# Performance work log

Measured on AMD Instinct MI355X. Metric: run time of the kernel, lower is better.

Reference implementation:

```python
import jax, jax.numpy as jnp
import numpy as np

N_NODES = 50000
N_EDGES = 500000
D_IN, D_HID = 128, 256


def _add_self_loops(edge_index, n):
    loop = jnp.arange(n, dtype=edge_index.dtype)
    src = jnp.concatenate([edge_index[0], loop])
    dst = jnp.concatenate([edge_index[1], loop])
    return src, dst


def _gcn_layer(x, W, b, src, dst, dinv_sqrt, n):
    # x: [N, d_in] -> h: [N, d_out]
    h = x @ W
    # symmetric normalization D^{-1/2} (A+I) D^{-1/2}
    norm = dinv_sqrt[src] * dinv_sqrt[dst]          # [E+N]
    msg = h[src] * norm[:, None]                    # gather + scale
    agg = jax.ops.segment_sum(msg, dst, num_segments=n)  # scatter-add
    return agg + b


def setup_inputs() -> dict:
    key = jax.random.key(0)
    ks = jax.random.split(key, 8)
    x = jax.random.normal(ks[0], (N_NODES, D_IN), dtype=jnp.float32)
    edge_index = jax.random.randint(ks[1], (2, N_EDGES), 0, N_NODES, dtype=jnp.int64 if jax.config.read('jax_enable_x64') else jnp.int32)
    s = lambda fan_in: 1.0 / np.sqrt(fan_in)
    W1 = jax.random.uniform(ks[2], (D_IN, D_HID), jnp.float32, -s(D_IN), s(D_IN))
    b1 = jnp.zeros((D_HID,), jnp.float32)
    W2 = jax.random.uniform(ks[3], (D_HID, D_HID), jnp.float32, -s(D_HID), s(D_HID))
    b2 = jnp.zeros((D_HID,), jnp.float32)
    W3 = jax.random.uniform(ks[4], (D_HID, D_HID), jnp.float32, -s(D_HID), s(D_HID))
    b3 = jnp.zeros((D_HID,), jnp.float32)
    return {"x": x, "edge_index": edge_index, "W1": W1, "b1": b1,
            "W2": W2, "b2": b2, "W3": W3, "b3": b3}


def reference(x, edge_index, W1, b1, W2, b2, W3, b3):
    n = x.shape[0]
    src, dst = _add_self_loops(edge_index, n)
    # degree includes self loops (edge weight 1), as in torch_geometric GCNConv
    deg = jax.ops.segment_sum(jnp.ones_like(dst, dtype=x.dtype), dst, num_segments=n)
    dinv_sqrt = jnp.where(deg > 0, jax.lax.rsqrt(jnp.maximum(deg, 1e-12)), 0.0)
    h = jax.nn.relu(_gcn_layer(x, W1, b1, src, dst, dinv_sqrt, n))
    h = jax.nn.relu(_gcn_layer(h, W2, b2, src, dst, dinv_sqrt, n))
    h = _gcn_layer(h, W3, b3, src, dst, dinv_sqrt, n)
    return h
```

## Files before the change

### kernel.cpp

```cpp
#include <hip/hip_runtime.h>

#define NNODES 50000
#define NEDGES 500000
#define DIN 128
#define DHID 256
#define MPAD 50048
#define NI4 12500
#define NSB 49

typedef unsigned short u16;
typedef __attribute__((ext_vector_type(8))) _Float16 half8;
typedef __attribute__((ext_vector_type(4))) float f32x4;

__device__ __forceinline__ u16 f2h(float f) {
  union { _Float16 h; u16 u; } v; v.h = (_Float16)f; return v.u;
}
__device__ __forceinline__ float h2f(unsigned int u) {
  union { _Float16 h; u16 u; } v; v.u = (u16)u; return (float)v.h;
}

#define GLDS16(g, l) __builtin_amdgcn_global_load_lds( \
    (const __attribute__((address_space(1))) void*)(g), \
    (__attribute__((address_space(3))) void*)(l), 16, 0, 0)

__global__ void k_zero_i32(int* __restrict__ p, int n) {
  int i = blockIdx.x * blockDim.x + threadIdx.x;
  if (i < n) p[i] = 0;
}

__global__ void k_hist(const int* __restrict__ dst, int* __restrict__ deg, int e) {
  int i = blockIdx.x * blockDim.x + threadIdx.x;
  if (i < e) atomicAdd(&deg[dst[i]], 1);
}

__global__ __launch_bounds__(256) void k_blocksum(const int* __restrict__ deg,
                                                  int* __restrict__ partials) {
  __shared__ int red[256];
  int tid = threadIdx.x;
  int t4 = blockIdx.x * 256 + tid;
  int sum = 0;
  if (t4 < NI4) {
    int4 v = ((const int4*)deg)[t4];
    sum = v.x + v.y + v.z + v.w;
  }
  red[tid] = sum;
  __syncthreads();
  for (int off = 128; off > 0; off >>= 1) {
    if (tid < off) red[tid] += red[tid + off];
    __syncthreads();
  }
  if (tid == 0) partials[blockIdx.x] = red[0];
}

__global__ __launch_bounds__(256) void k_scan2(int* __restrict__ deg,
                                               const int* __restrict__ partials,
                                               int* __restrict__ row_ptr,
                                               float* __restrict__ dinv) {
  __shared__ int sdata[256];
  __shared__ int sprefix;
  int tid = threadIdx.x, bid = blockIdx.x;
  int t4 = bid * 256 + tid;
  int4 v = make_int4(0, 0, 0, 0);
  if (t4 < NI4) v = ((const int4*)deg)[t4];
  int tsum = v.x + v.y + v.z + v.w;
  sdata[tid] = tsum;
  if (tid == 0) {
    int pre = 0;
    for (int b = 0; b < bid; ++b) pre += partials[b];
    sprefix = pre;
  }
  __syncthreads();
  for (int off = 1; off < 256; off <<= 1) {
    int val = (tid >= off) ? sdata[tid - off] : 0;
    __syncthreads();
    sdata[tid] += val;
    __syncthreads();
  }
  if (t4 < NI4) {
    int run = sdata[tid] - tsum + sprefix;
    int base = t4 * 4;
    float4 dv;
    dv.x = rsqrtf((float)v.x + 1.0f);
    dv.y = rsqrtf((float)v.y + 1.0f);
    dv.z = rsqrtf((float)v.z + 1.0f);
    dv.w = rsqrtf((float)v.w + 1.0f);
    *(float4*)(dinv + base) = dv;
    row_ptr[base + 0] = run; run += v.x;
    row_ptr[base + 1] = run; run += v.y;
    row_ptr[base + 2] = run; run += v.z;
    row_ptr[base + 3] = run; run += v.w;
    if (base + 4 == NNODES) row_ptr[NNODES] = run;
    ((int4*)deg)[t4] = make_int4(0, 0, 0, 0);
  }
}

__global__ void k_fill(const int* __restrict__ src, const int* __restrict__ dst,
                       const float* __restrict__ dinv, const int* __restrict__ row_ptr,
                       int* __restrict__ cursor, int* __restrict__ csr_src,
                       float* __restrict__ csr_nrm, int e) {
  int i = blockIdx.x * blockDim.x + threadIdx.x;
  if (i < e) {
    int d = dst[i], s = src[i];
    int pos = row_ptr[d] + atomicAdd(&cursor[d], 1);
    csr_src[pos] = s;
    csr_nrm[pos] = dinv[s] * dinv[d];
  }
}

__global__ void k_x2f16(const float* __restrict__ x, u16* __restrict__ xh, int total4) {
  int i = blockIdx.x * blockDim.x + threadIdx.x;
  if (i >= total4) return;
  float4 v = ((const float4*)x)[i];
  ushort4 o;
  o.x = f2h(v.x); o.y = f2h(v.y); o.z = f2h(v.z); o.w = f2h(v.w);
  ((ushort4*)xh)[i] = o;
}

__global__ void k_splitW3(const float* __restrict__ W1f, u16* __restrict__ P1,
                          const float* __restrict__ W2f, u16* __restrict__ P2,
                          const float* __restrict__ W3f, u16* __restrict__ P3) {
  int i = blockIdx.x * blockDim.x + threadIdx.x;
  const int s1 = DIN * 256, s2 = s1 + DHID * 256, s3 = s2 + DHID * 256;
  if (i >= s3) return;
  const float* W; u16* P; int li;
  if (i < s1)      { W = W1f; P = P1; li = i; }
  else if (i < s2) { W = W2f; P = P2; li = i - s1; }
  else             { W = W3f; P = P3; li = i - s2; }
  int k = li >> 8, n = li & 255;
  int t = k >> 5, q = (k >> 3) & 3, j = k & 7;
  int c = n >> 4, m = n & 15;
  int f = (c * 64 + q * 16 + m) * 8 + j;
  float w = W[li] * 256.0f;
  u16 hi = f2h(w);
  u16 lo = f2h(w - h2f(hi));
  P[(size_t)t * 16384 + f] = hi;
  P[(size_t)t * 16384 + 8192 + f] = lo;
}

template<int K, int EPI>
__global__ __launch_bounds__(256, 2) void k_fused(const u16* __restrict__ hf,
                                                  const float* __restrict__ dinv,
                                                  const int* __restrict__ row_ptr,
                                                  const int* __restrict__ csr_src,
                                                  const float* __restrict__ csr_nrm,
                                                  const u16* __restrict__ Bpk,
                                                  const float* __restrict__ bias,
                                                  u16* __restrict__ hf16,
                                                  float* __restrict__ outf) {
  __shared__ __align__(16) u16 As[64 * K];
  __shared__ __align__(16) u16 Bs[16384];

  {
    constexpr int GL = K / 8;
    constexpr int NGRP = 256 / GL;
    constexpr int RPG = 64 / NGRP;
    const int gg = threadIdx.x / GL;
    const int sub = threadIdx.x % GL;
    const int coff = sub * 8;
    const int nbase = blockIdx.x * 64;

    for (int k = 0; k < RPG; ++k) {
      const int row = gg + k * NGRP;
      const int node = nbase + row;
      float acc[8];
      if (node < NNODES) {
        float di = dinv[node];
        float s2 = di * di;
        {
          half8 v = *(const half8*)(hf + (size_t)node * K + coff);
#pragma unroll
          for (int j = 0; j < 8; ++j) acc[j] = s2 * (float)v[j];
        }
        const int p0 = row_ptr[node];
        const int p1 = row_ptr[node + 1];
        for (int e = p0; e < p1; e += 8) {
          int idx[8]; float w[8];
#pragma unroll
          for (int q = 0; q < 8; ++q) {
            int ii = (e + q < p1) ? e + q : p1 - 1;
            idx[q] = csr_src[ii];
            w[q] = (e + q < p1) ? csr_nrm[ii] : 0.0f;
          }
          half8 v[8];
#pragma unroll
          for (int q = 0; q < 8; ++q)
            v[q] = *(const half8*)(hf + (size_t)idx[q] * K + coff);
#pragma unroll
          for (int q = 0; q < 8; ++q)
#pragma unroll
            for (int j = 0; j < 8; ++j)
              acc[j] = fmaf(w[q], (float)v[q][j], acc[j]);
        }
      } else {
#pragma unroll
        for (int j = 0; j < 8; ++j) acc[j] = 0.0f;
      }
      const int wc = coff ^ ((row & 7) << 3);
      uint4 o;
      o.x = (unsigned)f2h(acc[0]) | ((unsigned)f2h(acc[1]) << 16);
      o.y = (unsigned)f2h(acc[2]) | ((unsigned)f2h(acc[3]) << 16);
      o.z = (unsigned)f2h(acc[4]) | ((unsigned)f2h(acc[5]) << 16);
      o.w = (unsigned)f2h(acc[6]) | ((unsigned)f2h(acc[7]) << 16);
      *(uint4*)&As[row * K + wc] = o;
    }
  }

  const int lane = threadIdx.x & 63;
  const int wave = threadIdx.x >> 6;
  const int rw = wave & 1, cw = wave >> 1;
  const int m0 = blockIdx.x * 64 + rw * 32;
  const int lr0 = rw * 32 + (lane & 15);
  const int lr1 = lr0 + 16;
  const int acoff = (lane >> 4) * 8;

  f32x4 acc0[8], acc1[8];
#pragma unroll
  for (int c = 0; c < 8; ++c) {
    acc0[c] = {0.f, 0.f, 0.f, 0.f};
    acc1[c] = {0.f, 0.f, 0.f, 0.f};
  }

  for (int t = 0; t < K / 32; ++t) {
    __syncthreads();
    {
      const char* gsrc = (const char*)(Bpk + (size_t)t * 16384);
      char* lbase = (char*)Bs;
#pragma unroll
      for (int it = 0; it < 8; ++it) {
        int off = (wave * 8 + it) * 1024 + lane * 16;
        GLDS16(gsrc + off, lbase + off);
      }
    }
    __syncthreads();

    const int ac = acoff + t * 32;
    half8 a0 = *(const half8*)&As[lr0 * K + (ac ^ ((lr0 & 7) << 3))];
    half8 a1 = *(const half8*)&As[lr1 * K + (ac ^ ((lr1 & 7) << 3))];
#pragma unroll
    for (int c = 0; c < 8; ++c) {
      const u16* fb = Bs + ((cw * 8 + c) * 64 + lane) * 8;
      half8 bh = *(const half8*)fb;
      half8 bl = *(const half8*)(fb + 8192);
      acc0[c] = __builtin_amdgcn_mfma_f32_16x16x32_f16(a0, bh, acc0[c], 0, 0, 0);
      acc0[c] = __builtin_amdgcn_mfma_f32_16x16x32_f16(a0, bl, acc0[c], 0, 0, 0);
      acc1[c] = __builtin_amdgcn_mfma_f32_16x16x32_f16(a1, bh, acc1[c], 0, 0, 0);
      acc1[c] = __builtin_amdgcn_mfma_f32_16x16x32_f16(a1, bl, acc1[c], 0, 0, 0);
    }
  }

  const int cbase = lane & 15;
  const int r0 = m0 + ((lane >> 4) * 4);
  const float sc = 1.0f / 256.0f;
#pragma unroll
  for (int c = 0; c < 8; ++c) {
    int col = (cw * 8 + c) * 16 + cbase;
    float bv = bias[col];
#pragma unroll
    for (int r = 0; r < 4; ++r) {
      float v0 = fmaf(acc0[c][r], sc, bv);
      float v1 = fmaf(acc1[c][r], sc, bv);
      if (EPI == 0) {
        v0 = fmaxf(v0, 0.f);
        v1 = fmaxf(v1, 0.f);
        hf16[(size_t)(r0 + r) * 256 + col] = f2h(v0);
        hf16[(size_t)(r0 + 16 + r) * 256 + col] = f2h(v1);
      } else {
        if (r0 + r < NNODES) outf[(size_t)(r0 + r) * 256 + col] = v0;
        if (r0 + 16 + r < NNODES) outf[(size_t)(r0 + 16 + r) * 256 + col] = v1;
      }
    }
  }
}

extern "C" void kernel_launch(void* const* d_in, const int* in_sizes, int n_in,
                              void* d_out, int out_size, void* d_ws, size_t ws_size,
                              hipStream_t stream) {
  const float* x  = (const float*)d_in[0];
  const int*   ei = (const int*)d_in[1];
  const float* W1 = (const float*)d_in[2];
  const float* b1 = (const float*)d_in[3];
  const float* W2 = (const float*)d_in[4];
  const float* b2 = (const float*)d_in[5];
  const float* W3 = (const float*)d_in[6];
  const float* b3 = (const float*)d_in[7];
  float* out = (float*)d_out;
  (void)in_sizes; (void)n_in; (void)out_size; (void)ws_size;

  char* ws = (char*)d_ws;
  size_t off = 0;
  auto alloc = [&](size_t bytes) -> void* {
    void* p = (void*)(ws + off);
    off += (bytes + 255) & ~(size_t)255;
    return p;
  };
  float* dinv    = (float*)alloc((size_t)NNODES * 4);
  int*   deg     = (int*)alloc((size_t)NNODES * 4);
  int*   row_ptr = (int*)alloc((size_t)(NNODES + 1) * 4);
  int*   partials= (int*)alloc((size_t)NSB * 4);
  int*   csr_src = (int*)alloc((size_t)NEDGES * 4);
  float* csr_nrm = (float*)alloc((size_t)NEDGES * 4);
  u16*   xh      = (u16*)alloc((size_t)NNODES * DIN * 2);
  u16*   hbufA   = (u16*)alloc((size_t)MPAD * 256 * 2);
  u16*   hbufB   = (u16*)alloc((size_t)MPAD * 256 * 2);
  u16*   W1pk    = (u16*)alloc((size_t)(DIN / 32) * 16384 * 2);
  u16*   W2pk    = (u16*)alloc((size_t)(DHID / 32) * 16384 * 2);
  u16*   W3pk    = (u16*)alloc((size_t)(DHID / 32) * 16384 * 2);

  const int* e_src = ei;
  const int* e_dst = ei + NEDGES;

  const int tb = 256;
  k_zero_i32<<<(NNODES + tb - 1) / tb, tb, 0, stream>>>(deg, NNODES);
  k_hist<<<(NEDGES + tb - 1) / tb, tb, 0, stream>>>(e_dst, deg, NEDGES);
  k_blocksum<<<NSB, 256, 0, stream>>>(deg, partials);
  k_scan2<<<NSB, 256, 0, stream>>>(deg, partials, row_ptr, dinv);
  k_fill<<<(NEDGES + tb - 1) / tb, tb, 0, stream>>>(e_src, e_dst, dinv, row_ptr, deg,
                                                    csr_src, csr_nrm, NEDGES);

  int x4 = NNODES * DIN / 4;
  k_x2f16<<<(x4 + tb - 1) / tb, tb, 0, stream>>>(x, xh, x4);
  int wtot = (DIN + DHID + DHID) * 256;
  k_splitW3<<<(wtot + tb - 1) / tb, tb, 0, stream>>>(W1, W1pk, W2, W2pk, W3, W3pk);

  const int gblocks = MPAD / 64;

  k_fused<DIN, 0><<<gblocks, 256, 0, stream>>>(xh, dinv, row_ptr, csr_src, csr_nrm,
                                               W1pk, b1, hbufA, nullptr);
  k_fused<DHID, 0><<<gblocks, 256, 0, stream>>>(hbufA, dinv, row_ptr, csr_src, csr_nrm,
                                                W2pk, b2, hbufB, nullptr);
  k_fused<DHID, 1><<<gblocks, 256, 0, stream>>>(hbufB, dinv, row_ptr, csr_src, csr_nrm,
                                                W3pk, b3, nullptr, out);
}
```

Baseline: 351.2 us.

## Read packed weights directly from global memory instead of staging in LDS

```diff
diff --git a/kernel.cpp b/kernel.cpp
--- a/kernel.cpp
+++ b/kernel.cpp
@@ -18,10 +18,6 @@
 __device__ __forceinline__ float h2f(unsigned int u) {
   union { _Float16 h; u16 u; } v; v.u = (u16)u; return (float)v.h;
 }
-
-#define GLDS16(g, l) __builtin_amdgcn_global_load_lds( \
-    (const __attribute__((address_space(1))) void*)(g), \
-    (__attribute__((address_space(3))) void*)(l), 16, 0, 0)
 
 __global__ void k_zero_i32(int* __restrict__ p, int n) {
   int i = blockIdx.x * blockDim.x + threadIdx.x;
@@ -107,38 +103,37 @@
   }
 }
 
-__global__ void k_x2f16(const float* __restrict__ x, u16* __restrict__ xh, int total4) {
+__global__ void k_prep(const float* __restrict__ x, u16* __restrict__ xh, int total4,
+                       const float* __restrict__ W1f, u16* __restrict__ P1,
+                       const float* __restrict__ W2f, u16* __restrict__ P2,
+                       const float* __restrict__ W3f, u16* __restrict__ P3) {
   int i = blockIdx.x * blockDim.x + threadIdx.x;
-  if (i >= total4) return;
-  float4 v = ((const float4*)x)[i];
-  ushort4 o;
-  o.x = f2h(v.x); o.y = f2h(v.y); o.z = f2h(v.z); o.w = f2h(v.w);
-  ((ushort4*)xh)[i] = o;
-}
-
-__global__ void k_splitW3(const float* __restrict__ W1f, u16* __restrict__ P1,
-                          const float* __restrict__ W2f, u16* __restrict__ P2,
-                          const float* __restrict__ W3f, u16* __restrict__ P3) {
-  int i = blockIdx.x * blockDim.x + threadIdx.x;
+  if (i < total4) {
+    float4 v = ((const float4*)x)[i];
+    ushort4 o;
+    o.x = f2h(v.x); o.y = f2h(v.y); o.z = f2h(v.z); o.w = f2h(v.w);
+    ((ushort4*)xh)[i] = o;
+  }
   const int s1 = DIN * 256, s2 = s1 + DHID * 256, s3 = s2 + DHID * 256;
-  if (i >= s3) return;
-  const float* W; u16* P; int li;
-  if (i < s1)      { W = W1f; P = P1; li = i; }
-  else if (i < s2) { W = W2f; P = P2; li = i - s1; }
-  else             { W = W3f; P = P3; li = i - s2; }
-  int k = li >> 8, n = li & 255;
-  int t = k >> 5, q = (k >> 3) & 3, j = k & 7;
-  int c = n >> 4, m = n & 15;
-  int f = (c * 64 + q * 16 + m) * 8 + j;
-  float w = W[li] * 256.0f;
-  u16 hi = f2h(w);
-  u16 lo = f2h(w - h2f(hi));
-  P[(size_t)t * 16384 + f] = hi;
-  P[(size_t)t * 16384 + 8192 + f] = lo;
+  if (i < s3) {
+    const float* W; u16* P; int li;
+    if (i < s1)      { W = W1f; P = P1; li = i; }
+    else if (i < s2) { W = W2f; P = P2; li = i - s1; }
+    else             { W = W3f; P = P3; li = i - s2; }
+    int k = li >> 8, n = li & 255;
+    int t = k >> 5, q = (k >> 3) & 3, j = k & 7;
+    int c = n >> 4, m = n & 15;
+    int f = (c * 64 + q * 16 + m) * 8 + j;
+    float w = W[li] * 256.0f;
+    u16 hi = f2h(w);
+    u16 lo = f2h(w - h2f(hi));
+    P[(size_t)t * 16384 + f] = hi;
+    P[(size_t)t * 16384 + 8192 + f] = lo;
+  }
 }
 
 template<int K, int EPI>
-__global__ __launch_bounds__(256, 2) void k_fused(const u16* __restrict__ hf,
+__global__ __launch_bounds__(256, 4) void k_fused(const u16* __restrict__ hf,
                                                   const float* __restrict__ dinv,
                                                   const int* __restrict__ row_ptr,
                                                   const int* __restrict__ csr_src,
@@ -148,7 +143,6 @@
                                                   u16* __restrict__ hf16,
                                                   float* __restrict__ outf) {
   __shared__ __align__(16) u16 As[64 * K];
-  __shared__ __align__(16) u16 Bs[16384];
 
   {
     constexpr int GL = K / 8;
@@ -205,6 +199,8 @@
     }
   }
 
+  __syncthreads();
+
   const int lane = threadIdx.x & 63;
   const int wave = threadIdx.x >> 6;
   const int rw = wave & 1, cw = wave >> 1;
@@ -221,24 +217,13 @@
   }
 
   for (int t = 0; t < K / 32; ++t) {
-    __syncthreads();
-    {
-      const char* gsrc = (const char*)(Bpk + (size_t)t * 16384);
-      char* lbase = (char*)Bs;
-#pragma unroll
-      for (int it = 0; it < 8; ++it) {
-        int off = (wave * 8 + it) * 1024 + lane * 16;
-        GLDS16(gsrc + off, lbase + off);
-      }
-    }
-    __syncthreads();
-
     const int ac = acoff + t * 32;
     half8 a0 = *(const half8*)&As[lr0 * K + (ac ^ ((lr0 & 7) << 3))];
     half8 a1 = *(const half8*)&As[lr1 * K + (ac ^ ((lr1 & 7) << 3))];
+    const u16* bt = Bpk + (size_t)t * 16384 + ((size_t)cw * 8 * 64 + lane) * 8;
 #pragma unroll
     for (int c = 0; c < 8; ++c) {
-      const u16* fb = Bs + ((cw * 8 + c) * 64 + lane) * 8;
+      const u16* fb = bt + c * 512;
       half8 bh = *(const half8*)fb;
       half8 bl = *(const half8*)(fb + 8192);
       acc0[c] = __builtin_amdgcn_mfma_f32_16x16x32_f16(a0, bh, acc0[c], 0, 0, 0);
@@ -318,9 +303,8 @@
                                                     csr_src, csr_nrm, NEDGES);
 
   int x4 = NNODES * DIN / 4;
-  k_x2f16<<<(x4 + tb - 1) / tb, tb, 0, stream>>>(x, xh, x4);
-  int wtot = (DIN + DHID + DHID) * 256;
-  k_splitW3<<<(wtot + tb - 1) / tb, tb, 0, stream>>>(W1, W1pk, W2, W2pk, W3, W3pk);
+  k_prep<<<(x4 + tb - 1) / tb, tb, 0, stream>>>(x, xh, x4,
+                                                W1, W1pk, W2, W2pk, W3, W3pk);
 
   const int gblocks = MPAD / 64;
 
```

After: 327.7 us. 1.07x faster.
